# Optimization experiments

Hardware: AMD Instinct MI355X
Metric: run time of the kernel (lower is better)

## Reference

```python
import jax, jax.numpy as jnp
import numpy as np

N_HEAD = 12
N_EMBD = 768

def setup_inputs() -> dict:
    key = jax.random.key(0)
    ks = jax.random.split(key, 5)
    B, T, C = 4, 2048, N_EMBD
    x = jax.random.normal(ks[0], (B, T, C), dtype=jnp.float32)
    # PyTorch Linear default init ~ U(-1/sqrt(fan_in), 1/sqrt(fan_in)); use small normals for a clean baseline
    s = 1.0 / np.sqrt(C)
    W_attn = jax.random.uniform(ks[1], (C, 3 * C), minval=-s, maxval=s, dtype=jnp.float32)
    b_attn = jax.random.uniform(ks[2], (3 * C,), minval=-s, maxval=s, dtype=jnp.float32)
    W_o = jax.random.uniform(ks[3], (C, C), minval=-s, maxval=s, dtype=jnp.float32)
    b_o = jax.random.uniform(ks[4], (C,), minval=-s, maxval=s, dtype=jnp.float32)
    return {"x": x, "W_attn": W_attn, "b_attn": b_attn, "W_o": W_o, "b_o": b_o}

def reference(x, W_attn, b_attn, W_o, b_o):
    B, T, C = x.shape
    H = N_HEAD
    D = C // H  # head dim
    qkv = x @ W_attn + b_attn                      # [B,T,3C]
    q, k, v = jnp.split(qkv, 3, axis=-1)           # each [B,T,C]
    q = q.reshape(B, T, H, D).transpose(0, 2, 1, 3)  # [B,H,T,D]
    k = k.reshape(B, T, H, D).transpose(0, 2, 1, 3)
    v = v.reshape(B, T, H, D).transpose(0, 2, 1, 3)
    att = jnp.einsum('bhqd,bhkd->bhqk', q, k) / jnp.sqrt(jnp.asarray(D, x.dtype))
    causal = jnp.tril(jnp.ones((T, T), dtype=bool))
    att = jnp.where(causal, att, jnp.asarray(-jnp.inf, att.dtype))
    att = jax.nn.softmax(att, axis=-1)             # dropout=0.0 -> identity
    y = jnp.einsum('bhqk,bhkd->bhqd', att, v)      # [B,H,T,D]
    y = y.transpose(0, 2, 1, 3).reshape(B, T, C)   # [B,T,C]
    return y @ W_o + b_o
```

## Files before the change

kernel.cpp:

```cpp
#include <hip/hip_runtime.h>
#include <hip/hip_bf16.h>

#define NHEAD 12
#define TSEQ 2048
#define CEMB 768
#define DHEAD 64
#define NBATCH 4

typedef __attribute__((ext_vector_type(8))) short bf16x8;
typedef __attribute__((ext_vector_type(4))) float f32x4;
typedef __attribute__((ext_vector_type(4))) unsigned u32x4;

template <int N> struct IC { static constexpr int value = N; };

__device__ __forceinline__ ushort f2bf(float f) {
  union { float f; unsigned u; } v; v.f = f;
  unsigned u = v.u;
  u += 0x7FFFu + ((u >> 16) & 1u);
  return (ushort)(u >> 16);
}

__device__ __forceinline__ unsigned cvt_pk_bf16(float lo, float hi) {
  unsigned r;
  asm("v_cvt_pk_bf16_f32 %0, %1, %2" : "=v"(r) : "v"(lo), "v"(hi));
  return r;
}

__device__ __forceinline__ float exp2_raw(float x) {
  float r;
  asm("v_exp_f32 %0, %1" : "=v"(r) : "v"(x));
  return r;
}

__device__ __forceinline__ void permswap32(unsigned& a, unsigned& b) {
  asm("v_permlane32_swap_b32 %0, %1" : "+v"(a), "+v"(b));
}
__device__ __forceinline__ void permswap16(unsigned& a, unsigned& b) {
  asm("v_permlane16_swap_b32 %0, %1" : "+v"(a), "+v"(b));
}

__global__ __launch_bounds__(256)
void prep(const float* __restrict__ x, ushort* __restrict__ xb,
          const float* __restrict__ Wa, ushort* __restrict__ WaT,
          const float* __restrict__ Wo, ushort* __restrict__ WoT)
{
  __shared__ float tile[32][33];
  const int bid = blockIdx.x, t = threadIdx.x;
  if (bid < 3072) {
    int i = (bid * 256 + t) * 8;
    float4 v0 = *(const float4*)(x + i);
    float4 v1 = *(const float4*)(x + i + 4);
    bf16x8 wv;
    wv[0] = (short)f2bf(v0.x); wv[1] = (short)f2bf(v0.y);
    wv[2] = (short)f2bf(v0.z); wv[3] = (short)f2bf(v0.w);
    wv[4] = (short)f2bf(v1.x); wv[5] = (short)f2bf(v1.y);
    wv[6] = (short)f2bf(v1.z); wv[7] = (short)f2bf(v1.w);
    *(bf16x8*)(xb + i) = wv;
    return;
  }
  const int b2 = bid - 3072;
  const int bx = b2 % 96, by = b2 / 96;
  const int tx = t & 31, ty = t >> 5;
  const float* src; ushort* dst; int C, c0;
  if (bx < 72) { src = Wa; dst = WaT; C = 3 * CEMB; c0 = bx * 32; }
  else         { src = Wo; dst = WoT; C = CEMB;     c0 = (bx - 72) * 32; }
  const int r0 = by * 32;
#pragma unroll
  for (int j = 0; j < 4; ++j)
    tile[ty + j * 8][tx] = src[(size_t)(r0 + ty + j * 8) * C + c0 + tx];
  __syncthreads();
#pragma unroll
  for (int j = 0; j < 4; ++j)
    dst[(size_t)(c0 + ty + j * 8) * CEMB + r0 + tx] = f2bf(tile[tx][ty + j * 8]);
}

template<int EPI>
__global__ __launch_bounds__(256)
void gemm_bf16(const ushort* __restrict__ A, const ushort* __restrict__ BT,
               const float* __restrict__ bias, float* __restrict__ outF,
               ushort* __restrict__ qd, ushort* __restrict__ kd, ushort* __restrict__ vd,
               int M, int N, int K)
{
  __shared__ __align__(16) char smem[49152];
  const int t = threadIdx.x;
  const int lane = t & 63, wv = t >> 6;
  const int cc = lane & 15, gg = lane >> 4;
  const int nN = N >> 7, nM = M >> 7;
  const int L = blockIdx.x;
  const int xcd = L & 7, li = L >> 3;
  const int mi = li / nN + (nM >> 3) * xcd;
  const int ni = li % nN;
  const int m0 = mi * 128, n0 = ni * 128;
  const int wm = (wv >> 1) * 64, wn = (wv & 1) * 64;

  const int o0 = wv * 1024 + lane * 16;
  const int o1 = o0 + 4096;
  const int r0s = o0 >> 6, s0s = (o0 >> 4) & 3;
  const int r1s = o1 >> 6, s1s = (o1 >> 4) & 3;
  const size_t Kb = (size_t)K * 2;
  const char* a0p = (const char*)A  + (size_t)(m0 + r0s) * Kb + ((s0s ^ ((r0s >> 1) & 3)) << 4);
  const char* a1p = (const char*)A  + (size_t)(m0 + r1s) * Kb + ((s1s ^ ((r1s >> 1) & 3)) << 4);
  const char* b0p = (const char*)BT + (size_t)(n0 + r0s) * Kb + ((s0s ^ ((r0s >> 1) & 3)) << 4);
  const char* b1p = (const char*)BT + (size_t)(n0 + r1s) * Kb + ((s1s ^ ((r1s >> 1) & 3)) << 4);

  auto stage_g = [&](int p, int kb) {
    char* As = smem + p * 16384;
    char* Bs = As + 8192;
    __builtin_amdgcn_global_load_lds(
        (const __attribute__((address_space(1))) unsigned*)(a0p + kb),
        (__attribute__((address_space(3))) unsigned*)(As + wv * 1024), 16, 0, 0);
    __builtin_amdgcn_global_load_lds(
        (const __attribute__((address_space(1))) unsigned*)(a1p + kb),
        (__attribute__((address_space(3))) unsigned*)(As + wv * 1024 + 4096), 16, 0, 0);
    __builtin_amdgcn_global_load_lds(
        (const __attribute__((address_space(1))) unsigned*)(b0p + kb),
        (__attribute__((address_space(3))) unsigned*)(Bs + wv * 1024), 16, 0, 0);
    __builtin_amdgcn_global_load_lds(
        (const __attribute__((address_space(1))) unsigned*)(b1p + kb),
        (__attribute__((address_space(3))) unsigned*)(Bs + wv * 1024 + 4096), 16, 0, 0);
  };

  f32x4 acc[4][4];
#pragma unroll
  for (int i = 0; i < 4; ++i)
#pragma unroll
    for (int j = 0; j < 4; ++j) acc[i][j] = (f32x4){0.f, 0.f, 0.f, 0.f};

  const int NK = (K * 2) / 64;
  stage_g(0, 0);
  stage_g(1, 64);
  asm volatile("s_waitcnt vmcnt(4)" ::: "memory");
  __builtin_amdgcn_s_barrier();
  __builtin_amdgcn_sched_barrier(0);

  for (int ik = 0; ik < NK; ++ik) {
    const bool pre = (ik + 2 < NK);
    if (pre) stage_g((ik + 2) % 3, (ik + 2) * 64);
    const char* As = smem + (ik % 3) * 16384;
    const char* Bs = As + 8192;
    bf16x8 fa[4], fb[4];
#pragma unroll
    for (int i = 0; i < 4; ++i) {
      const int r = wm + i * 16 + cc;
      fa[i] = *(const bf16x8*)(As + r * 64 + ((gg ^ ((r >> 1) & 3)) << 4));
    }
#pragma unroll
    for (int j = 0; j < 4; ++j) {
      const int r = wn + j * 16 + cc;
      fb[j] = *(const bf16x8*)(Bs + r * 64 + ((gg ^ ((r >> 1) & 3)) << 4));
    }
    __builtin_amdgcn_s_setprio(1);
#pragma unroll
    for (int i = 0; i < 4; ++i)
#pragma unroll
      for (int j = 0; j < 4; ++j)
        acc[i][j] = __builtin_amdgcn_mfma_f32_16x16x32_bf16(fa[i], fb[j], acc[i][j], 0, 0, 0);
    __builtin_amdgcn_s_setprio(0);
    if (ik + 1 < NK) {
      if (pre) asm volatile("s_waitcnt vmcnt(4)" ::: "memory");
      else     asm volatile("s_waitcnt vmcnt(0)" ::: "memory");
      __builtin_amdgcn_s_barrier();
      __builtin_amdgcn_sched_barrier(0);
    }
  }

#pragma unroll
  for (int i = 0; i < 4; ++i) {
#pragma unroll
    for (int j = 0; j < 4; ++j) {
      int gm0 = m0 + wm + i * 16 + gg * 4;
      int gn  = n0 + wn + j * 16 + cc;
      float bv = bias[gn];
      if (EPI == 0) {
#pragma unroll
        for (int e = 0; e < 4; ++e)
          outF[(size_t)(gm0 + e) * N + gn] = acc[i][j][e] + bv;
      } else {
        int which = gn / CEMB;
        int r = gn - which * CEMB;
        int hh = r >> 6, dd = r & 63;
        int tt0 = gm0 & (TSEQ - 1), bb = gm0 >> 11;
        if (which == 2) {
          ushort* dstv = vd + ((size_t)((bb * NHEAD + hh) * DHEAD + dd)) * TSEQ + tt0;
          uint2 pw;
          pw.x = cvt_pk_bf16(acc[i][j][0] + bv, acc[i][j][1] + bv);
          pw.y = cvt_pk_bf16(acc[i][j][2] + bv, acc[i][j][3] + bv);
          *(uint2*)dstv = pw;
        } else {
          ushort* dst = which == 0 ? qd : kd;
          float sc = (which == 0) ? 0.125f * 1.4426950408889634f : 1.0f;
#pragma unroll
          for (int e = 0; e < 4; ++e)
            dst[(size_t)((bb * NHEAD + hh) * TSEQ + tt0 + e) * DHEAD + dd] =
                f2bf((acc[i][j][e] + bv) * sc);
        }
      }
    }
  }
}

__global__ __launch_bounds__(256, 5)
void attn_fwd(const ushort* __restrict__ qg, const ushort* __restrict__ kg,
              const ushort* __restrict__ vTg, ushort* __restrict__ ybb)
{
  __shared__ __align__(16) char smem[32768];
  const int t = threadIdx.x, lane = t & 63, w = t >> 6;
  const int cc = lane & 15, gg = lane >> 4;
  const int L = blockIdx.x;
  const int slot = L & 7, j = L >> 3;
  const int qt = 31 - j / 6;
  const int bh = slot + 8 * (j % 6);
  const int b = bh / NHEAD, h = bh - b * NHEAD;

  const char* Kg = (const char*)(kg + (size_t)bh * TSEQ * DHEAD);
  const char* Vg = (const char*)(vTg + (size_t)bh * TSEQ * DHEAD);

  const int srow = lane >> 3;
  const int ssw  = ((lane & 7) * 16) ^ (srow << 4);

  const int g16s = (gg * 16) ^ ((cc & 7) << 4);
  const char* lb0 = smem + cc * 128 + g16s;
  const char* lb1 = smem + cc * 128 + (g16s ^ 64);

  bf16x8 ones;
#pragma unroll
  for (int i = 0; i < 8; ++i) ones[i] = (short)0x3F80;

  auto stageK = [&](int pb, int kt) {
#pragma unroll
    for (int i = 0; i < 2; ++i) {
      const int c = w * 2 + i;
      const char* gk = Kg + (size_t)(kt * 64 + c * 8 + srow) * 128 + ssw;
      __builtin_amdgcn_global_load_lds(
          (const __attribute__((address_space(1))) unsigned*)gk,
          (__attribute__((address_space(3))) unsigned*)(smem + pb * 8192 + c * 1024),
          16, 0, 0);
    }
  };
  auto stageV = [&](int pb, int kt) {
#pragma unroll
    for (int i = 0; i < 2; ++i) {
      const int c = w * 2 + i;
      const char* gv = Vg + (size_t)(c * 8 + srow) * (TSEQ * 2) + (size_t)kt * 128 + ssw;
      __builtin_amdgcn_global_load_lds(
          (const __attribute__((address_space(1))) unsigned*)gv,
          (__attribute__((address_space(3))) unsigned*)(smem + 16384 + pb * 8192 + c * 1024),
          16, 0, 0);
    }
  };

  const int qrow0 = qt * 64 + w * 16;

  const ushort* Qp = qg + ((size_t)bh * TSEQ + qrow0) * DHEAD;
  bf16x8 fq0 = *(const bf16x8*)(Qp + cc * DHEAD + 8 * gg);
  bf16x8 fq1 = *(const bf16x8*)(Qp + cc * DHEAD + 32 + 8 * gg);

  f32x4 o[4];
  f32x4 l4 = (f32x4){0.f, 0.f, 0.f, 0.f};
#pragma unroll
  for (int i = 0; i < 4; ++i) o[i] = (f32x4){0.f, 0.f, 0.f, 0.f};
  float m = 0.f;
  u32x4 pbf[2];
  pbf[0] = (u32x4){0, 0, 0, 0}; pbf[1] = (u32x4){0, 0, 0, 0};

  stageK(0, 0);
  asm volatile("s_waitcnt vmcnt(0)" ::: "memory");
  __syncthreads();

  auto tile = [&](auto PC, int kt) {
    constexpr int P = decltype(PC)::value;
    if (kt < qt) stageK(P ^ 1, kt + 1);
    stageV(P, kt);

    f32x4 st[4];
#pragma unroll
    for (int ct = 0; ct < 4; ++ct) st[ct] = (f32x4){0.f, 0.f, 0.f, 0.f};
    __builtin_amdgcn_s_setprio(1);
#pragma unroll
    for (int ct = 0; ct < 4; ++ct) {
      bf16x8 fk0 = *(const bf16x8*)(lb0 + P * 8192 + ct * 2048);
      bf16x8 fk1 = *(const bf16x8*)(lb1 + P * 8192 + ct * 2048);
      st[ct] = __builtin_amdgcn_mfma_f32_16x16x32_bf16(fk0, fq0, st[ct], 0, 0, 0);
      st[ct] = __builtin_amdgcn_mfma_f32_16x16x32_bf16(fk1, fq1, st[ct], 0, 0, 0);
    }

    if (kt > 0) {
#pragma unroll
      for (int kc = 0; kc < 2; ++kc) {
        bf16x8 pb = __builtin_bit_cast(bf16x8, pbf[kc]);
        l4 = __builtin_amdgcn_mfma_f32_16x16x32_bf16(ones, pb, l4, 0, 0, 0);
        const char* vb = (kc == 0) ? lb0 : lb1;
#pragma unroll
        for (int dt = 0; dt < 4; ++dt) {
          bf16x8 fv = *(const bf16x8*)(vb + 16384 + (P ^ 1) * 8192 + dt * 2048);
          o[dt] = __builtin_amdgcn_mfma_f32_16x16x32_bf16(fv, pb, o[dt], 0, 0, 0);
        }
      }
    }
    __builtin_amdgcn_s_setprio(0);

    if (kt == qt) {
#pragma unroll
      for (int ct = 0; ct < 4; ++ct)
#pragma unroll
        for (int e = 0; e < 4; ++e)
          if (ct * 16 + gg * 4 + e > w * 16 + cc) st[ct][e] = -1e30f;
    }
    f32x4 pe[4];
#pragma unroll
    for (int ct = 0; ct < 4; ++ct)
#pragma unroll
      for (int e = 0; e < 4; ++e) pe[ct][e] = exp2_raw(st[ct][e] - m);
    float ml = fmaxf(fmaxf(st[0][0], st[0][1]), st[0][2]);
    ml = fmaxf(fmaxf(ml, st[0][3]), fmaxf(st[1][0], st[1][1]));
    ml = fmaxf(fmaxf(ml, st[1][2]), fmaxf(st[1][3], st[2][0]));
    ml = fmaxf(fmaxf(ml, st[2][1]), fmaxf(st[2][2], st[2][3]));
    ml = fmaxf(fmaxf(ml, st[3][0]), fmaxf(st[3][1], st[3][2]));
    ml = fmaxf(ml, st[3][3]);
    if (!__all(ml - m <= 11.54f)) {
      ml = fmaxf(ml, __shfl_xor(ml, 16, 64));
      ml = fmaxf(ml, __shfl_xor(ml, 32, 64));
      ml = fmaxf(ml, __shfl_xor(ml, 1, 64));
      ml = fmaxf(ml, __shfl_xor(ml, 2, 64));
      ml = fmaxf(ml, __shfl_xor(ml, 4, 64));
      ml = fmaxf(ml, __shfl_xor(ml, 8, 64));
      float mn = fmaxf(m, ml);
      float al = exp2_raw(m - mn);
#pragma unroll
      for (int dt = 0; dt < 4; ++dt)
#pragma unroll
        for (int e = 0; e < 4; ++e) o[dt][e] *= al;
#pragma unroll
      for (int e = 0; e < 4; ++e) l4[e] *= al;
#pragma unroll
      for (int ct = 0; ct < 4; ++ct)
#pragma unroll
        for (int e = 0; e < 4; ++e) pe[ct][e] *= al;
      m = mn;
    }
    {
      unsigned X0 = cvt_pk_bf16(pe[0][0], pe[0][1]), X1 = cvt_pk_bf16(pe[0][2], pe[0][3]);
      unsigned Y0 = cvt_pk_bf16(pe[1][0], pe[1][1]), Y1 = cvt_pk_bf16(pe[1][2], pe[1][3]);
      unsigned Z0 = cvt_pk_bf16(pe[2][0], pe[2][1]), Z1 = cvt_pk_bf16(pe[2][2], pe[2][3]);
      unsigned W0 = cvt_pk_bf16(pe[3][0], pe[3][1]), W1 = cvt_pk_bf16(pe[3][2], pe[3][3]);
      permswap32(X0, Y0); permswap16(X0, Y0);
      permswap32(X1, Y1); permswap16(X1, Y1);
      permswap32(Z0, W0); permswap16(Z0, W0);
      permswap32(Z1, W1); permswap16(Z1, W1);
      pbf[0] = (u32x4){X0, X1, Y0, Y1};
      pbf[1] = (u32x4){Z0, Z1, W0, W1};
    }

    asm volatile("s_waitcnt vmcnt(0)" ::: "memory");
    __syncthreads();
  };

  for (int kt = 0; kt <= qt; kt += 2) {
    tile(IC<0>{}, kt);
    if (kt + 1 <= qt) tile(IC<1>{}, kt + 1);
  }

  {
    const int pl = qt & 1;
#pragma unroll
    for (int kc = 0; kc < 2; ++kc) {
      bf16x8 pb = __builtin_bit_cast(bf16x8, pbf[kc]);
      l4 = __builtin_amdgcn_mfma_f32_16x16x32_bf16(ones, pb, l4, 0, 0, 0);
      const char* vb = (kc == 0) ? lb0 : lb1;
#pragma unroll
      for (int dt = 0; dt < 4; ++dt) {
        bf16x8 fv = *(const bf16x8*)(vb + 16384 + pl * 8192 + dt * 2048);
        o[dt] = __builtin_amdgcn_mfma_f32_16x16x32_bf16(fv, pb, o[dt], 0, 0, 0);
      }
    }
  }

  float inv = 1.0f / l4[0];
  ushort* yrow = ybb + (size_t)(b * TSEQ + qrow0 + cc) * CEMB + h * DHEAD;
#pragma unroll
  for (int dt = 0; dt < 4; ++dt) {
    uint2 pw;
    pw.x = cvt_pk_bf16(o[dt][0] * inv, o[dt][1] * inv);
    pw.y = cvt_pk_bf16(o[dt][2] * inv, o[dt][3] * inv);
    *(uint2*)(yrow + dt * 16 + gg * 4) = pw;
  }
}

extern "C" void kernel_launch(void* const* d_in, const int* in_sizes, int n_in,
                              void* d_out, int out_size, void* d_ws, size_t ws_size,
                              hipStream_t stream)
{
  (void)in_sizes; (void)n_in; (void)out_size; (void)ws_size;
  const float* x  = (const float*)d_in[0];
  const float* Wa = (const float*)d_in[1];
  const float* ba = (const float*)d_in[2];
  const float* Wo = (const float*)d_in[3];
  const float* bo = (const float*)d_in[4];
  float* out = (float*)d_out;

  char* p = (char*)d_ws;
  ushort* WaT  = (ushort*)p; p += (size_t)3 * CEMB * CEMB * 2;
  ushort* WoT  = (ushort*)p; p += (size_t)CEMB * CEMB * 2;
  ushort* xb   = (ushort*)p; p += (size_t)NBATCH * TSEQ * CEMB * 2;
  ushort* qb   = (ushort*)p; p += (size_t)NBATCH * NHEAD * TSEQ * DHEAD * 2;
  ushort* kb   = (ushort*)p; p += (size_t)NBATCH * NHEAD * TSEQ * DHEAD * 2;
  ushort* vT   = (ushort*)p; p += (size_t)NBATCH * NHEAD * TSEQ * DHEAD * 2;
  ushort* yb   = (ushort*)p; p += (size_t)NBATCH * TSEQ * CEMB * 2;

  prep<<<3072 + 96 * 24, 256, 0, stream>>>(x, xb, Wa, WaT, Wo, WoT);
  gemm_bf16<1><<<dim3((NBATCH * TSEQ / 128) * (3 * CEMB / 128)), 256, 0, stream>>>(
      xb, WaT, ba, nullptr, qb, kb, vT, NBATCH * TSEQ, 3 * CEMB, CEMB);
  attn_fwd<<<dim3(1536), 256, 0, stream>>>(qb, kb, vT, yb);
  gemm_bf16<0><<<dim3((NBATCH * TSEQ / 128) * (CEMB / 128)), 256, 0, stream>>>(
      yb, WoT, bo, out, nullptr, nullptr, nullptr, NBATCH * TSEQ, CEMB, CEMB);
}
```

Before: 115.0 us.

## Use 256x128 tiles with 512-thread blocks for the QKV projection GEMM

Splits the QKV projection into its own kernel that uses 512-thread blocks computing 256x128 output tiles, so each staged B tile is shared by eight waves instead of four. The kernel double-buffers global-to-LDS loads with a simpler wait-all-then-barrier loop and maps blocks to XCDs by M strip. The goal is to halve B-operand traffic per output and cut the block count for the largest GEMM. In exchange it waits on all outstanding loads every iteration, which drops the finer vmcnt pipelining of the old kernel, and it uses more LDS and registers per block. The output projection GEMM stays as before under a new name.

```diff
diff --git a/kernel.cpp b/kernel.cpp
--- a/kernel.cpp
+++ b/kernel.cpp
@@ -74,12 +74,117 @@
     dst[(size_t)(c0 + ty + j * 8) * CEMB + r0 + tx] = f2bf(tile[tx][ty + j * 8]);
 }
 
-template<int EPI>
+__global__ __launch_bounds__(512, 6)
+void gemm_qkv(const ushort* __restrict__ A, const ushort* __restrict__ BT,
+              const float* __restrict__ bias,
+              ushort* __restrict__ qd, ushort* __restrict__ kd, ushort* __restrict__ vd,
+              int M, int N, int K)
+{
+  __shared__ __align__(16) char smem[49152];
+  const int t = threadIdx.x;
+  const int lane = t & 63, wv = t >> 6;
+  const int cc = lane & 15, gg = lane >> 4;
+  const int L = blockIdx.x;
+  const int xcd = L & 7, li = L >> 3;
+  const int mi = xcd * 4 + (li & 3);
+  const int ni = li >> 2;
+  const int m0 = mi * 256, n0 = ni * 128;
+  const int wm = (wv >> 1) * 64, wn = (wv & 1) * 64;
+
+  const int o0 = t * 16;
+  const int o1 = 8192 + t * 16;
+  const int r0s = o0 >> 6, s0s = (o0 >> 4) & 3;
+  const int r1s = o1 >> 6, s1s = (o1 >> 4) & 3;
+  const size_t Kb = (size_t)K * 2;
+  const char* a0p = (const char*)A  + (size_t)(m0 + r0s) * Kb + ((s0s ^ ((r0s >> 1) & 3)) << 4);
+  const char* a1p = (const char*)A  + (size_t)(m0 + r1s) * Kb + ((s1s ^ ((r1s >> 1) & 3)) << 4);
+  const char* b0p = (const char*)BT + (size_t)(n0 + r0s) * Kb + ((s0s ^ ((r0s >> 1) & 3)) << 4);
+
+  auto stage_g = [&](int p, int kb) {
+    char* As = smem + p * 24576;
+    char* Bs = As + 16384;
+    __builtin_amdgcn_global_load_lds(
+        (const __attribute__((address_space(1))) unsigned*)(a0p + kb),
+        (__attribute__((address_space(3))) unsigned*)(As + wv * 1024), 16, 0, 0);
+    __builtin_amdgcn_global_load_lds(
+        (const __attribute__((address_space(1))) unsigned*)(a1p + kb),
+        (__attribute__((address_space(3))) unsigned*)(As + 8192 + wv * 1024), 16, 0, 0);
+    __builtin_amdgcn_global_load_lds(
+        (const __attribute__((address_space(1))) unsigned*)(b0p + kb),
+        (__attribute__((address_space(3))) unsigned*)(Bs + wv * 1024), 16, 0, 0);
+  };
+
+  f32x4 acc[4][4];
+#pragma unroll
+  for (int i = 0; i < 4; ++i)
+#pragma unroll
+    for (int j = 0; j < 4; ++j) acc[i][j] = (f32x4){0.f, 0.f, 0.f, 0.f};
+
+  const int KB = K * 2;
+  stage_g(0, 0);
+  asm volatile("s_waitcnt vmcnt(0)" ::: "memory");
+  __syncthreads();
+  int p = 0;
+  for (int kb = 0; kb < KB; kb += 64) {
+    if (kb + 64 < KB) stage_g(p ^ 1, kb + 64);
+    const char* As = smem + p * 24576;
+    const char* Bs = As + 16384;
+    bf16x8 fa[4], fb[4];
+#pragma unroll
+    for (int i = 0; i < 4; ++i) {
+      const int r = wm + i * 16 + cc;
+      fa[i] = *(const bf16x8*)(As + r * 64 + ((gg ^ ((r >> 1) & 3)) << 4));
+    }
+#pragma unroll
+    for (int j = 0; j < 4; ++j) {
+      const int r = wn + j * 16 + cc;
+      fb[j] = *(const bf16x8*)(Bs + r * 64 + ((gg ^ ((r >> 1) & 3)) << 4));
+    }
+    __builtin_amdgcn_s_setprio(1);
+#pragma unroll
+    for (int i = 0; i < 4; ++i)
+#pragma unroll
+      for (int j = 0; j < 4; ++j)
+        acc[i][j] = __builtin_amdgcn_mfma_f32_16x16x32_bf16(fa[i], fb[j], acc[i][j], 0, 0, 0);
+    __builtin_amdgcn_s_setprio(0);
+    asm volatile("s_waitcnt vmcnt(0)" ::: "memory");
+    __syncthreads();
+    p ^= 1;
+  }
+
+#pragma unroll
+  for (int i = 0; i < 4; ++i) {
+#pragma unroll
+    for (int j = 0; j < 4; ++j) {
+      int gm0 = m0 + wm + i * 16 + gg * 4;
+      int gn  = n0 + wn + j * 16 + cc;
+      float bv = bias[gn];
+      int which = gn / CEMB;
+      int r = gn - which * CEMB;
+      int hh = r >> 6, dd = r & 63;
+      int tt0 = gm0 & (TSEQ - 1), bb = gm0 >> 11;
+      if (which == 2) {
+        ushort* dstv = vd + ((size_t)((bb * NHEAD + hh) * DHEAD + dd)) * TSEQ + tt0;
+        uint2 pw;
+        pw.x = cvt_pk_bf16(acc[i][j][0] + bv, acc[i][j][1] + bv);
+        pw.y = cvt_pk_bf16(acc[i][j][2] + bv, acc[i][j][3] + bv);
+        *(uint2*)dstv = pw;
+      } else {
+        ushort* dst = which == 0 ? qd : kd;
+        float sc = (which == 0) ? 0.125f * 1.4426950408889634f : 1.0f;
+#pragma unroll
+        for (int e = 0; e < 4; ++e)
+          dst[(size_t)((bb * NHEAD + hh) * TSEQ + tt0 + e) * DHEAD + dd] =
+              f2bf((acc[i][j][e] + bv) * sc);
+      }
+    }
+  }
+}
+
 __global__ __launch_bounds__(256)
-void gemm_bf16(const ushort* __restrict__ A, const ushort* __restrict__ BT,
-               const float* __restrict__ bias, float* __restrict__ outF,
-               ushort* __restrict__ qd, ushort* __restrict__ kd, ushort* __restrict__ vd,
-               int M, int N, int K)
+void gemm_out(const ushort* __restrict__ A, const ushort* __restrict__ BT,
+              const float* __restrict__ bias, float* __restrict__ outF,
+              int M, int N, int K)
 {
   __shared__ __align__(16) char smem[49152];
   const int t = threadIdx.x;
@@ -171,30 +276,9 @@
       int gm0 = m0 + wm + i * 16 + gg * 4;
       int gn  = n0 + wn + j * 16 + cc;
       float bv = bias[gn];
-      if (EPI == 0) {
-#pragma unroll
-        for (int e = 0; e < 4; ++e)
-          outF[(size_t)(gm0 + e) * N + gn] = acc[i][j][e] + bv;
-      } else {
-        int which = gn / CEMB;
-        int r = gn - which * CEMB;
-        int hh = r >> 6, dd = r & 63;
-        int tt0 = gm0 & (TSEQ - 1), bb = gm0 >> 11;
-        if (which == 2) {
-          ushort* dstv = vd + ((size_t)((bb * NHEAD + hh) * DHEAD + dd)) * TSEQ + tt0;
-          uint2 pw;
-          pw.x = cvt_pk_bf16(acc[i][j][0] + bv, acc[i][j][1] + bv);
-          pw.y = cvt_pk_bf16(acc[i][j][2] + bv, acc[i][j][3] + bv);
-          *(uint2*)dstv = pw;
-        } else {
-          ushort* dst = which == 0 ? qd : kd;
-          float sc = (which == 0) ? 0.125f * 1.4426950408889634f : 1.0f;
-#pragma unroll
-          for (int e = 0; e < 4; ++e)
-            dst[(size_t)((bb * NHEAD + hh) * TSEQ + tt0 + e) * DHEAD + dd] =
-                f2bf((acc[i][j][e] + bv) * sc);
-        }
-      }
+#pragma unroll
+      for (int e = 0; e < 4; ++e)
+        outF[(size_t)(gm0 + e) * N + gn] = acc[i][j][e] + bv;
     }
   }
 }
@@ -408,9 +492,9 @@
   ushort* yb   = (ushort*)p; p += (size_t)NBATCH * TSEQ * CEMB * 2;
 
   prep<<<3072 + 96 * 24, 256, 0, stream>>>(x, xb, Wa, WaT, Wo, WoT);
-  gemm_bf16<1><<<dim3((NBATCH * TSEQ / 128) * (3 * CEMB / 128)), 256, 0, stream>>>(
-      xb, WaT, ba, nullptr, qb, kb, vT, NBATCH * TSEQ, 3 * CEMB, CEMB);
+  gemm_qkv<<<dim3((NBATCH * TSEQ / 256) * (3 * CEMB / 128)), 512, 0, stream>>>(
+      xb, WaT, ba, qb, kb, vT, NBATCH * TSEQ, 3 * CEMB, CEMB);
   attn_fwd<<<dim3(1536), 256, 0, stream>>>(qb, kb, vT, yb);
-  gemm_bf16<0><<<dim3((NBATCH * TSEQ / 128) * (CEMB / 128)), 256, 0, stream>>>(
-      yb, WoT, bo, out, nullptr, nullptr, nullptr, NBATCH * TSEQ, CEMB, CEMB);
-}
+  gemm_out<<<dim3((NBATCH * TSEQ / 128) * (CEMB / 128)), 256, 0, stream>>>(
+      yb, WoT, bo, out, NBATCH * TSEQ, CEMB, CEMB);
+}
```

Result: slower. 343.4 us (+198.5%).
